# Performance work log

Hardware: AMD Instinct MI355X
Metric: run time of the kernel (lower is better)

Reference implementation:

```python
import jax, jax.numpy as jnp
import numpy as np

T, B, D, N, C, I = 512, 128, 3, 512, 2, 1


def setup_inputs() -> dict:
    key = jax.random.key(0)
    ks = jax.random.split(key, 12)
    s_hh = 1.0 / np.sqrt(N)
    return {
        "data": jax.random.normal(ks[0], (T, B, I), jnp.float32),
        "h0": 0.1 * jax.random.uniform(ks[1], (D, B, N), jnp.float32),
        "W_in": jax.random.normal(ks[2], (D, N, I), jnp.float32),
        "b_in": 0.1 * jax.random.normal(ks[3], (D, N), jnp.float32),
        "W_hh": s_hh * jax.random.normal(ks[4], (D, N, N), jnp.float32),
        "b_hh": 0.1 * jax.random.normal(ks[5], (D, N), jnp.float32),
        "W_ff": s_hh * jax.random.normal(ks[6], (D - 1, N, N), jnp.float32),
        "b_ff": 0.1 * jax.random.normal(ks[7], (D - 1, N), jnp.float32),
        "taus": 1.0 + jax.random.uniform(ks[8], (D, N), jnp.float32),
        "W_fc": s_hh * jax.random.normal(ks[9], (D, C, N), jnp.float32),
        "b_fc": 0.1 * jax.random.normal(ks[10], (D, C), jnp.float32),
    }


def reference(data, h0, W_in, b_in, W_hh, b_hh, W_ff, b_ff, taus, W_fc, b_fc):
    D_ = W_hh.shape[0]
    # recurrent weights have their diagonal zeroed before the time loop
    Whh = W_hh * (1.0 - jnp.eye(W_hh.shape[-1], dtype=W_hh.dtype))
    # precompute input projections for all timesteps: [T, D, B, N]
    x_all = jnp.einsum('tbi,dni->tdbn', data, W_in) + b_in[None, :, None, :]
    tau_c = jnp.maximum(taus, 1.0)            # clamp(tau, min=1.0), [D, N]
    alpha = 1.0 - 1.0 / tau_c                 # decay factor
    inv_tau = 1.0 / tau_c

    def step(h, x_t):  # h: [D, B, N], x_t: [D, B, N]
        new = []
        for d in range(D_):
            pre = h[d] @ Whh[d].T + b_hh[d] + x_t[d]
            if d > 0:
                # hierarchical signal uses the already-updated lower module state
                pre = pre + new[d - 1] @ W_ff[d - 1].T + b_ff[d - 1]
            h_new = alpha[d] * h[d] + jax.nn.leaky_relu(pre) * inv_tau[d]
            new.append(h_new)
        return jnp.stack(new), None

    h_final, _ = jax.lax.scan(step, h0, x_all)
    # per-module readout heads on final hidden state: [D, B, C]
    out = jnp.einsum('dbn,dcn->dbc', h_final, W_fc) + b_fc[:, None, :]
    return h_final, out
```

## Files before the change

kernel.cpp:

```cpp
#include <hip/hip_runtime.h>


#define TSTEPS 512
#define BATCH  128
#define DMOD   3
#define NH     512
#define CCLS   2
#define OUT2   (DMOD * BATCH * NH)
#define LSBPAT 0x0001000100010001ULL

typedef unsigned long long u64;
typedef unsigned int u32;
typedef __attribute__((ext_vector_type(8))) short bf16x8;
typedef __attribute__((ext_vector_type(4))) float f32x4;

__device__ __forceinline__ float bflo(u32 u) { return __uint_as_float(u << 16); }
__device__ __forceinline__ float bfhi(u32 u) { return __uint_as_float(u & 0xffff0000u); }
__device__ __forceinline__ unsigned short f2bf(float x) {
    u32 u = __float_as_uint(x);
    return (unsigned short)((u + 0x7fffu + ((u >> 16) & 1u)) >> 16);
}
__device__ __forceinline__ u64 pack4bf(float a, float b, float c, float d) {
    u32 lo = (u32)f2bf(a) | ((u32)f2bf(b) << 16);
    u32 hi = (u32)f2bf(c) | ((u32)f2bf(d) << 16);
    return (u64)lo | ((u64)hi << 32);
}
__device__ __forceinline__ float lrelu(float x) { return fmaxf(x, 0.01f * x); }

__device__ __forceinline__ u64 ld_h(const u64* p) {
    return __hip_atomic_load(p, __ATOMIC_RELAXED, __HIP_MEMORY_SCOPE_AGENT);
}
__device__ __forceinline__ void st_h(u64* p, u64 v) {
    __hip_atomic_store(p, v, __ATOMIC_RELAXED, __HIP_MEMORY_SCOPE_AGENT);
}
__device__ __forceinline__ int ld_slot(const int* p) {
    return __hip_atomic_load(p, __ATOMIC_RELAXED, __HIP_MEMORY_SCOPE_AGENT);
}
__device__ __forceinline__ void st_slot(int* p, int v) {
    __hip_atomic_store(p, v, __ATOMIC_RELAXED, __HIP_MEMORY_SCOPE_AGENT);
}

__global__ __launch_bounds__(512, 2)
void rnn_mfma(const float* __restrict__ data,
              const float* __restrict__ h0,
              const float* __restrict__ W_in,
              const float* __restrict__ b_in,
              const float* __restrict__ W_hh,
              const float* __restrict__ b_hh,
              const float* __restrict__ W_ff,
              const float* __restrict__ b_ff,
              const float* __restrict__ taus,
              const float* __restrict__ W_fc,
              const float* __restrict__ b_fc,
              float* __restrict__ out,
              int* __restrict__ wsI)
{
    const int wgid = blockIdx.x;
    const int d    = wgid >> 5;
    const int rr   = wgid & 31;
    const int bt   = rr >> 2;
    const int q    = rr & 3;
    const int w    = threadIdx.x >> 6;
    const int lane = threadIdx.x & 63;
    const int nt   = q * 8 + w;
    const int colb = lane & 15;
    const int quad = lane >> 4;
    const int b    = bt * 16 + colb;
    const int n0   = nt * 16 + quad * 4;

    int* rdfl = wsI + 1024;
    u64* slab = (u64*)((char*)wsI + 65536);
    u64* fin  = slab + ((size_t)12 << 14);

    __shared__ u64 lsO[2048];
    __shared__ u64 lsF[2048];

    bf16x8 wOwn[16], wFf[16];
    {
        const int nrow = nt * 16 + colb;
        const float* gw = W_hh + ((size_t)d * NH + nrow) * NH;
        for (int kc = 0; kc < 16; ++kc) {
            int k0 = kc * 32 + quad * 8;
            union { unsigned short s[8]; bf16x8 v; } u;
            for (int j = 0; j < 8; ++j) {
                float x = gw[k0 + j];
                if (k0 + j == nrow) x = 0.f;
                u.s[j] = f2bf(x);
            }
            wOwn[kc] = u.v;
        }
        if (d > 0) {
            const float* gf = W_ff + ((size_t)(d - 1) * NH + nrow) * NH;
            for (int kc = 0; kc < 16; ++kc) {
                int k0 = kc * 32 + quad * 8;
                union { unsigned short s[8]; bf16x8 v; } u;
                for (int j = 0; j < 8; ++j) u.s[j] = f2bf(gf[k0 + j]);
                wFf[kc] = u.v;
            }
        }
    }

    float wi4[4], cb4[4], al4[4], it4[4];
#pragma unroll
    for (int k = 0; k < 4; ++k) {
        int n = n0 + k;
        wi4[k] = W_in[d * NH + n];
        float cbv = b_hh[d * NH + n] + b_in[d * NH + n];
        if (d > 0) cbv += b_ff[(d - 1) * NH + n];
        cb4[k] = cbv;
        float tc = fmaxf(taus[d * NH + n], 1.0f);
        it4[k] = 1.0f / tc;
        al4[k] = 1.0f - it4[k];
    }

    const int cohBaseR = d * 32 + bt * 4;
    const int l3 = lane & 3;
    int* rmy = rdfl + cohBaseR + q;
    const int* rOwn = rdfl + cohBaseR + l3;
    const int* rUp  = rdfl + (d < DMOD - 1 ? cohBaseR + 32 : cohBaseR) + l3;

    const int scol = threadIdx.x & 127;
    const int sr0  = threadIdx.x >> 7;
    const int cA   = scol ^ (sr0 << 1);
    const int cB   = scol ^ ((sr0 + 4) << 1);

    u64 prev = 0;

    for (int t = 0; t < TSTEPS; ++t) {
        if (t == 0) {
            const float* hp = h0 + ((size_t)(d * BATCH) + bt * 16) * NH;
            float4 x0 = *(const float4*)(hp + (size_t)(sr0     ) * NH + scol * 4);
            float4 x1 = *(const float4*)(hp + (size_t)(sr0 +  4) * NH + scol * 4);
            float4 x2 = *(const float4*)(hp + (size_t)(sr0 +  8) * NH + scol * 4);
            float4 x3 = *(const float4*)(hp + (size_t)(sr0 + 12) * NH + scol * 4);
            lsO[(sr0     ) * 128 + cA] = pack4bf(x0.x, x0.y, x0.z, x0.w);
            lsO[(sr0 +  4) * 128 + cB] = pack4bf(x1.x, x1.y, x1.z, x1.w);
            lsO[(sr0 +  8) * 128 + cA] = pack4bf(x2.x, x2.y, x2.z, x2.w);
            lsO[(sr0 + 12) * 128 + cB] = pack4bf(x3.x, x3.y, x3.z, x3.w);
        } else {
            const u64* sp = slab + (((size_t)((t - 1) & 3) * 3 + d) << 14)
                          + (size_t)(bt * 16) * 128 + scol;
            const u64 ex = (((((t - 1) >> 2) & 1) ^ 1) != 0) ? LSBPAT : 0ULL;
            u64 v0, v1, v2, v3;
            while (1) {
                v0 = ld_h(sp + (size_t)(sr0     ) * 128);
                v1 = ld_h(sp + (size_t)(sr0 +  4) * 128);
                v2 = ld_h(sp + (size_t)(sr0 +  8) * 128);
                v3 = ld_h(sp + (size_t)(sr0 + 12) * 128);
                u64 bad = ((v0 ^ ex) | (v1 ^ ex) | (v2 ^ ex) | (v3 ^ ex)) & LSBPAT;
                if (__all(bad == 0)) break;
                __builtin_amdgcn_s_sleep(1);
            }
            lsO[(sr0     ) * 128 + cA] = v0;
            lsO[(sr0 +  4) * 128 + cB] = v1;
            lsO[(sr0 +  8) * 128 + cA] = v2;
            lsO[(sr0 + 12) * 128 + cB] = v3;
        }
        if (d > 0) {
            const u64* gp = slab + (((size_t)(t & 3) * 3 + (d - 1)) << 14)
                          + (size_t)(bt * 16) * 128 + scol;
            const u64 ex = ((((t >> 2) & 1) ^ 1) != 0) ? LSBPAT : 0ULL;
            u64 v0, v1, v2, v3;
            while (1) {
                v0 = ld_h(gp + (size_t)(sr0     ) * 128);
                v1 = ld_h(gp + (size_t)(sr0 +  4) * 128);
                v2 = ld_h(gp + (size_t)(sr0 +  8) * 128);
                v3 = ld_h(gp + (size_t)(sr0 + 12) * 128);
                u64 bad = ((v0 ^ ex) | (v1 ^ ex) | (v2 ^ ex) | (v3 ^ ex)) & LSBPAT;
                if (__all(bad == 0)) break;
                __builtin_amdgcn_s_sleep(1);
            }
            lsF[(sr0     ) * 128 + cA] = v0;
            lsF[(sr0 +  4) * 128 + cB] = v1;
            lsF[(sr0 +  8) * 128 + cA] = v2;
            lsF[(sr0 + 12) * 128 + cB] = v3;
        }
        float xs = data[t * BATCH + b];
        __syncthreads();
        if (w == 0 && lane == 0) st_slot(rmy, t);

        f32x4 acc = {0.f, 0.f, 0.f, 0.f};
        const int swz = (colb & 7) << 1;
        const int cq  = quad * 2;
        const u64* bO = lsO + (size_t)colb * 128;
#pragma unroll
        for (int kc = 0; kc < 16; ++kc) {
            bf16x8 bv = *(const bf16x8*)(bO + (((kc * 8 + cq) ^ swz)));
            acc = __builtin_amdgcn_mfma_f32_16x16x32_bf16(wOwn[kc], bv, acc, 0, 0, 0);
        }
        if (d > 0) {
            const u64* bF = lsF + (size_t)colb * 128;
#pragma unroll
            for (int kc = 0; kc < 16; ++kc) {
                bf16x8 bv = *(const bf16x8*)(bF + (((kc * 8 + cq) ^ swz)));
                acc = __builtin_amdgcn_mfma_f32_16x16x32_bf16(wFf[kc], bv, acc, 0, 0, 0);
            }
        }

        float h0f, h1f, h2f, h3f;
        if (t == 0) {
            float4 v = *(const float4*)(h0 + ((size_t)(d * BATCH) + b) * NH + n0);
            h0f = v.x; h1f = v.y; h2f = v.z; h3f = v.w;
        } else {
            h0f = bflo((u32)prev);         h1f = bfhi((u32)prev);
            h2f = bflo((u32)(prev >> 32)); h3f = bfhi((u32)(prev >> 32));
        }
        float p0 = acc.x + cb4[0] + xs * wi4[0];
        float p1 = acc.y + cb4[1] + xs * wi4[1];
        float p2 = acc.z + cb4[2] + xs * wi4[2];
        float p3 = acc.w + cb4[3] + xs * wi4[3];
        float n0v = al4[0] * h0f + lrelu(p0) * it4[0];
        float n1v = al4[1] * h1f + lrelu(p1) * it4[1];
        float n2v = al4[2] * h2f + lrelu(p2) * it4[2];
        float n3v = al4[3] * h3f + lrelu(p3) * it4[3];
        u64 pk = pack4bf(n0v, n1v, n2v, n3v);
        pk = (pk & ~LSBPAT) | ((((t >> 2) & 1) ^ 1) != 0 ? LSBPAT : 0ULL);
        prev = pk;

        if (w == 0 && t >= 4) {
            while (1) {
                bool ok = true;
                if (lane < 4) ok = (ld_slot(rOwn) >= t - 3);
                else if (lane < 8) { if (d < DMOD - 1) ok = (ld_slot(rUp) >= t - 4); }
                if (__all(ok)) break;
                __builtin_amdgcn_s_sleep(1);
            }
        }
        __syncthreads();

        st_h(slab + (((size_t)(t & 3) * 3 + d) << 14)
             + (size_t)b * 128 + (size_t)nt * 4 + quad, pk);
        if (t == TSTEPS - 1) {
            *(float4*)(out + ((size_t)(d * BATCH) + b) * NH + n0)
                = make_float4(n0v, n1v, n2v, n3v);
            st_h(fin + ((size_t)d << 14) + (size_t)b * 128 + (size_t)nt * 4 + quad,
                 pk | LSBPAT);
        }
    }

    if (q == 0 && w == 0 && lane < 32) {
        const int bb = bt * 16 + (lane & 15);
        const int c  = (lane >> 4) & 1;
        const u64* hf = fin + ((size_t)d << 14) + (size_t)bb * 128;
        const float4* wf = (const float4*)(W_fc + ((size_t)(d * CCLS) + c) * NH);
        float s = b_fc[d * CCLS + c];
        for (int q2 = 0; q2 < 128; ++q2) {
            u64 u;
            while (((u = ld_h(hf + q2)) & LSBPAT) != LSBPAT)
                __builtin_amdgcn_s_sleep(1);
            float4 ww = wf[q2];
            s += bflo((u32)u) * ww.x + bfhi((u32)u) * ww.y
               + bflo((u32)(u >> 32)) * ww.z + bfhi((u32)(u >> 32)) * ww.w;
        }
        out[OUT2 + (size_t)(d * BATCH + bb) * CCLS + c] = s;
    }
}

extern "C" void kernel_launch(void* const* d_in, const int* in_sizes, int n_in,
                              void* d_out, int out_size, void* d_ws, size_t ws_size,
                              hipStream_t stream) {
    const float* data = (const float*)d_in[0];
    const float* h0   = (const float*)d_in[1];
    const float* W_in = (const float*)d_in[2];
    const float* b_in = (const float*)d_in[3];
    const float* W_hh = (const float*)d_in[4];
    const float* b_hh = (const float*)d_in[5];
    const float* W_ff = (const float*)d_in[6];
    const float* b_ff = (const float*)d_in[7];
    const float* taus = (const float*)d_in[8];
    const float* W_fc = (const float*)d_in[9];
    const float* b_fc = (const float*)d_in[10];

    hipLaunchKernelGGL(rnn_mfma, dim3(96), dim3(512), 0, stream,
                       data, h0, W_in, b_in, W_hh, b_hh, W_ff, b_ff,
                       taus, W_fc, b_fc, (float*)d_out, (int*)d_ws);
}
```

Before: 1.686 ms.

## Double-buffer LDS hidden state, forward own slice locally, drop second barrier

Hidden-state and feed-forward staging in LDS is now double-buffered by timestep parity. This removes the end-of-step __syncthreads and moves the wave-0 slot-readiness spin to the start of the step, before the loads and the single barrier. Each workgroup writes its own freshly computed slice straight into the next step's LDS buffer, and loads only the other workgroups' slices from the global slab. The aim is less barrier and polling latency per step on the serial recurrence critical path, at the cost of twice the LDS footprint.

Result: slower. 1.816 ms (+7.7%).

```diff
diff --git a/kernel.cpp b/kernel.cpp
--- a/kernel.cpp
+++ b/kernel.cpp
@@ -72,8 +72,8 @@
     u64* slab = (u64*)((char*)wsI + 65536);
     u64* fin  = slab + ((size_t)12 << 14);
 
-    __shared__ u64 lsO[2048];
-    __shared__ u64 lsF[2048];
+    __shared__ u64 lsO[2][2048];
+    __shared__ u64 lsF[2][2048];
 
     bf16x8 wOwn[16], wFf[16];
     {
@@ -123,23 +123,38 @@
     const int sr0  = threadIdx.x >> 7;
     const int cA   = scol ^ (sr0 << 1);
     const int cB   = scol ^ ((sr0 + 4) << 1);
+    const size_t rowBase = (size_t)(bt * 16) * 128 + scol;
+    const bool isSelf = ((scol >> 5) == q);
+    const int selfIx = colb * 128 + ((nt * 4 + quad) ^ ((colb & 7) << 1));
 
     u64 prev = 0;
 
     for (int t = 0; t < TSTEPS; ++t) {
+        float xs = data[t * BATCH + b];
+
+        if (w == 0 && t >= 4) {
+            while (1) {
+                bool ok = true;
+                if (lane < 4) ok = (ld_slot(rOwn) >= t - 3);
+                else if (lane < 8) { if (d < DMOD - 1) ok = (ld_slot(rUp) >= t - 4); }
+                if (__all(ok)) break;
+                __builtin_amdgcn_s_sleep(1);
+            }
+        }
+
+        u64* oB = lsO[t & 1];
         if (t == 0) {
             const float* hp = h0 + ((size_t)(d * BATCH) + bt * 16) * NH;
             float4 x0 = *(const float4*)(hp + (size_t)(sr0     ) * NH + scol * 4);
             float4 x1 = *(const float4*)(hp + (size_t)(sr0 +  4) * NH + scol * 4);
             float4 x2 = *(const float4*)(hp + (size_t)(sr0 +  8) * NH + scol * 4);
             float4 x3 = *(const float4*)(hp + (size_t)(sr0 + 12) * NH + scol * 4);
-            lsO[(sr0     ) * 128 + cA] = pack4bf(x0.x, x0.y, x0.z, x0.w);
-            lsO[(sr0 +  4) * 128 + cB] = pack4bf(x1.x, x1.y, x1.z, x1.w);
-            lsO[(sr0 +  8) * 128 + cA] = pack4bf(x2.x, x2.y, x2.z, x2.w);
-            lsO[(sr0 + 12) * 128 + cB] = pack4bf(x3.x, x3.y, x3.z, x3.w);
-        } else {
-            const u64* sp = slab + (((size_t)((t - 1) & 3) * 3 + d) << 14)
-                          + (size_t)(bt * 16) * 128 + scol;
+            oB[(sr0     ) * 128 + cA] = pack4bf(x0.x, x0.y, x0.z, x0.w);
+            oB[(sr0 +  4) * 128 + cB] = pack4bf(x1.x, x1.y, x1.z, x1.w);
+            oB[(sr0 +  8) * 128 + cA] = pack4bf(x2.x, x2.y, x2.z, x2.w);
+            oB[(sr0 + 12) * 128 + cB] = pack4bf(x3.x, x3.y, x3.z, x3.w);
+        } else if (!isSelf) {
+            const u64* sp = slab + (((size_t)((t - 1) & 3) * 3 + d) << 14) + rowBase;
             const u64 ex = (((((t - 1) >> 2) & 1) ^ 1) != 0) ? LSBPAT : 0ULL;
             u64 v0, v1, v2, v3;
             while (1) {
@@ -151,45 +166,44 @@
                 if (__all(bad == 0)) break;
                 __builtin_amdgcn_s_sleep(1);
             }
-            lsO[(sr0     ) * 128 + cA] = v0;
-            lsO[(sr0 +  4) * 128 + cB] = v1;
-            lsO[(sr0 +  8) * 128 + cA] = v2;
-            lsO[(sr0 + 12) * 128 + cB] = v3;
+            oB[(sr0     ) * 128 + cA] = v0;
+            oB[(sr0 +  4) * 128 + cB] = v1;
+            oB[(sr0 +  8) * 128 + cA] = v2;
+            oB[(sr0 + 12) * 128 + cB] = v3;
         }
         if (d > 0) {
-            const u64* gp = slab + (((size_t)(t & 3) * 3 + (d - 1)) << 14)
-                          + (size_t)(bt * 16) * 128 + scol;
+            u64* fB = lsF[t & 1];
+            const u64* gp = slab + (((size_t)(t & 3) * 3 + (d - 1)) << 14) + rowBase;
             const u64 ex = ((((t >> 2) & 1) ^ 1) != 0) ? LSBPAT : 0ULL;
-            u64 v0, v1, v2, v3;
+            u64 g0, g1, g2, g3;
             while (1) {
-                v0 = ld_h(gp + (size_t)(sr0     ) * 128);
-                v1 = ld_h(gp + (size_t)(sr0 +  4) * 128);
-                v2 = ld_h(gp + (size_t)(sr0 +  8) * 128);
-                v3 = ld_h(gp + (size_t)(sr0 + 12) * 128);
-                u64 bad = ((v0 ^ ex) | (v1 ^ ex) | (v2 ^ ex) | (v3 ^ ex)) & LSBPAT;
+                g0 = ld_h(gp + (size_t)(sr0     ) * 128);
+                g1 = ld_h(gp + (size_t)(sr0 +  4) * 128);
+                g2 = ld_h(gp + (size_t)(sr0 +  8) * 128);
+                g3 = ld_h(gp + (size_t)(sr0 + 12) * 128);
+                u64 bad = ((g0 ^ ex) | (g1 ^ ex) | (g2 ^ ex) | (g3 ^ ex)) & LSBPAT;
                 if (__all(bad == 0)) break;
                 __builtin_amdgcn_s_sleep(1);
             }
-            lsF[(sr0     ) * 128 + cA] = v0;
-            lsF[(sr0 +  4) * 128 + cB] = v1;
-            lsF[(sr0 +  8) * 128 + cA] = v2;
-            lsF[(sr0 + 12) * 128 + cB] = v3;
-        }
-        float xs = data[t * BATCH + b];
+            fB[(sr0     ) * 128 + cA] = g0;
+            fB[(sr0 +  4) * 128 + cB] = g1;
+            fB[(sr0 +  8) * 128 + cA] = g2;
+            fB[(sr0 + 12) * 128 + cB] = g3;
+        }
         __syncthreads();
         if (w == 0 && lane == 0) st_slot(rmy, t);
 
         f32x4 acc = {0.f, 0.f, 0.f, 0.f};
         const int swz = (colb & 7) << 1;
         const int cq  = quad * 2;
-        const u64* bO = lsO + (size_t)colb * 128;
+        const u64* bO = oB + (size_t)colb * 128;
 #pragma unroll
         for (int kc = 0; kc < 16; ++kc) {
             bf16x8 bv = *(const bf16x8*)(bO + (((kc * 8 + cq) ^ swz)));
             acc = __builtin_amdgcn_mfma_f32_16x16x32_bf16(wOwn[kc], bv, acc, 0, 0, 0);
         }
         if (d > 0) {
-            const u64* bF = lsF + (size_t)colb * 128;
+            const u64* bF = lsF[t & 1] + (size_t)colb * 128;
 #pragma unroll
             for (int kc = 0; kc < 16; ++kc) {
                 bf16x8 bv = *(const bf16x8*)(bF + (((kc * 8 + cq) ^ swz)));
@@ -217,19 +231,9 @@
         pk = (pk & ~LSBPAT) | ((((t >> 2) & 1) ^ 1) != 0 ? LSBPAT : 0ULL);
         prev = pk;
 
-        if (w == 0 && t >= 4) {
-            while (1) {
-                bool ok = true;
-                if (lane < 4) ok = (ld_slot(rOwn) >= t - 3);
-                else if (lane < 8) { if (d < DMOD - 1) ok = (ld_slot(rUp) >= t - 4); }
-                if (__all(ok)) break;
-                __builtin_amdgcn_s_sleep(1);
-            }
-        }
-        __syncthreads();
-
         st_h(slab + (((size_t)(t & 3) * 3 + d) << 14)
              + (size_t)b * 128 + (size_t)nt * 4 + quad, pk);
+        lsO[(t + 1) & 1][selfIx] = pk;
         if (t == TSTEPS - 1) {
             *(float4*)(out + ((size_t)(d * BATCH) + b) * NH + n0)
                 = make_float4(n0v, n1v, n2v, n3v);
```
